# Kernel optimization log

Hardware: AMD Instinct MI355X
Metric: run time of the kernel (lower is better)

## Reference

```python
import jax, jax.numpy as jnp
import numpy as np

B, S, D = 2, 2048, 1024
H, K = 16, 64  # num_heads, n_hidden per head


def setup_inputs() -> dict:
    key = jax.random.key(0)
    ks = jax.random.split(key, 10)
    sc = 1.0 / np.sqrt(D)
    x = jax.random.normal(ks[0], (B, S, D), dtype=jnp.float32)
    attn_mask = jax.random.randint(ks[1], (B, S, S), 0, 2, dtype=jnp.int32)
    # per-head nn.Linear(d_input, n_hidden) weights stacked over heads: [H, D, K]
    W_Q = jax.random.normal(ks[2], (H, D, K), dtype=jnp.float32) * sc
    b_Q = jax.random.normal(ks[3], (H, K), dtype=jnp.float32) * sc
    W_K = jax.random.normal(ks[4], (H, D, K), dtype=jnp.float32) * sc
    b_K = jax.random.normal(ks[5], (H, K), dtype=jnp.float32) * sc
    W_V = jax.random.normal(ks[6], (H, D, K), dtype=jnp.float32) * sc
    b_V = jax.random.normal(ks[7], (H, K), dtype=jnp.float32) * sc
    # output projection nn.Linear(H*K, D)
    W_proj = jax.random.normal(ks[8], (H * K, D), dtype=jnp.float32) / np.sqrt(H * K)
    b_proj = jax.random.normal(ks[9], (D,), dtype=jnp.float32) / np.sqrt(H * K)
    return {"x": x, "W_Q": W_Q, "b_Q": b_Q, "W_K": W_K, "b_K": b_K,
            "W_V": W_V, "b_V": b_V, "W_proj": W_proj, "b_proj": b_proj,
            "attn_mask": attn_mask}


def reference(x, W_Q, b_Q, W_K, b_K, W_V, b_V, W_proj, b_proj, attn_mask):
    # Q/K/V for all heads at once: [B, H, S, K]
    Q = jnp.einsum('bsd,hdk->bhsk', x, W_Q) + b_Q[None, :, None, :]
    Kt = jnp.einsum('bsd,hdk->bhsk', x, W_K) + b_K[None, :, None, :]
    V = jnp.einsum('bsd,hdk->bhsk', x, W_V) + b_V[None, :, None, :]
    scale = 1.0 / np.sqrt(K).astype(np.float32)
    scores = jnp.einsum('bhsk,bhtk->bhst', Q, Kt) * scale  # [B,H,S,S]
    neg_inf = jnp.finfo(scores.dtype).min
    scores = jnp.where(attn_mask[:, None, :, :] == 0, neg_inf, scores)
    attn_scores = jax.nn.softmax(scores, axis=-1)  # [B,H,S,S]
    heads = jnp.einsum('bhst,bhtk->bhsk', attn_scores, V)  # [B,H,S,K]
    # concat heads along feature dim -> [B, S, H*K]
    concat = heads.transpose(0, 2, 1, 3).reshape(B, S, H * K)
    attn_output = concat @ W_proj + b_proj  # [B, S, D]
    return attn_output, attn_scores
```

## Files before the change

### kernel.cpp

```cpp
#include <hip/hip_runtime.h>

typedef unsigned short u16;
typedef unsigned int u32;
typedef unsigned long long u64;
typedef __attribute__((ext_vector_type(8))) short short8;
typedef __attribute__((ext_vector_type(8))) float float8;
typedef __attribute__((ext_vector_type(4))) float floatx4;

__device__ __forceinline__ u16 f2bf(float f) {
    unsigned u = __float_as_uint(f);
    return (u16)((u + 0x7FFFu + ((u >> 16) & 1u)) >> 16);
}

#define MFMA(a, b, c) __builtin_amdgcn_mfma_f32_16x16x32_bf16((a), (b), (c), 0, 0, 0)

#define AST 40
#define KST 72
#define C2 0.18033688011112043f

__global__ __launch_bounds__(256) void k_wtall(
    const float* __restrict__ wq, const float* __restrict__ wk,
    const float* __restrict__ wv, const float* __restrict__ wp,
    u16* __restrict__ wt3, u16* __restrict__ wpT)
{
    int slot = blockIdx.x >> 9;
    int id = (blockIdx.x & 511) * 256 + threadIdx.x;
    const float* in; u16* out; int logC;
    if (slot == 3) { in = wp; out = wpT; logC = 10; }
    else {
        in = (slot == 0) ? wq : (slot == 1 ? wk : wv);
        out = wt3 + (size_t)slot * 1048576;
        logC = 6;
    }
    int rg = id & 127;
    int rest = id >> 7;
    int C = 1 << logC;
    int cc = rest & (C - 1);
    int bt = rest >> logC;
    const float* src = in + ((size_t)bt << (10 + logC)) + cc;
    int r0 = rg * 8;
    short8 o;
    #pragma unroll
    for (int j = 0; j < 8; j++) o[j] = (short)f2bf(src[(size_t)(r0 + j) << logC]);
    *(short8*)&out[(((size_t)bt << logC) + cc) * 1024 + r0] = o;
}

__global__ __launch_bounds__(256) void k_projqkv(
    const float* __restrict__ x,
    const float* __restrict__ wq, const float* __restrict__ bq,
    const float* __restrict__ wk, const float* __restrict__ bk,
    const float* __restrict__ wv, const float* __restrict__ bv,
    const u16* __restrict__ wtT,
    u16* __restrict__ Qout, u16* __restrict__ Kout, u16* __restrict__ Vout)
{
    int mt = blockIdx.x, h = blockIdx.y;
    int tid = threadIdx.x, wave = tid >> 6, lane = tid & 63;
    int col = lane & 15, quad = lane >> 4, m0 = wave * 16;
    int rg0 = mt * 64;
    bool doQ = (Qout != nullptr);

    __shared__ __align__(16) char pool[4 * 64 * AST * 2];
    u16* As = (u16*)pool;
    u16* Bq = As + 64 * AST;
    u16* Bk = Bq + 64 * AST;
    u16* Bv = Bk + 64 * AST;

    floatx4 aQ[4], aK[4], aV[4];
    for (int i = 0; i < 4; i++) { aQ[i] = (floatx4){0,0,0,0}; aK[i] = (floatx4){0,0,0,0}; aV[i] = (floatx4){0,0,0,0}; }

    int lr = tid >> 2, lc = (tid & 3) * 8;
    float8 av = *(const float8*)&x[(size_t)(rg0 + lr) * 1024 + lc];

    if (wtT) {
        const u16* wqT = wtT + ((size_t)h * 64) * 1024;
        const u16* wkT = wqT + 1048576;
        const u16* wvT = wkT + 1048576;
        int nr = tid >> 2, dc = (tid & 3) * 8;
        short8 q8 = *(const short8*)&wqT[(size_t)nr * 1024 + dc];
        short8 k8 = *(const short8*)&wkT[(size_t)nr * 1024 + dc];
        short8 v8 = *(const short8*)&wvT[(size_t)nr * 1024 + dc];
        for (int dk = 0; dk < 1024; dk += 32) {
            short8 a8;
            #pragma unroll
            for (int j = 0; j < 8; j++) a8[j] = (short)f2bf(av[j]);
            *(short8*)&As[lr * AST + lc] = a8;
            *(short8*)&Bq[nr * AST + dc] = q8;
            *(short8*)&Bk[nr * AST + dc] = k8;
            *(short8*)&Bv[nr * AST + dc] = v8;
            __syncthreads();
            if (dk + 32 < 1024) {
                av = *(const float8*)&x[(size_t)(rg0 + lr) * 1024 + dk + 32 + lc];
                q8 = *(const short8*)&wqT[(size_t)nr * 1024 + dk + 32 + dc];
                k8 = *(const short8*)&wkT[(size_t)nr * 1024 + dk + 32 + dc];
                v8 = *(const short8*)&wvT[(size_t)nr * 1024 + dk + 32 + dc];
            }
            short8 a = *(const short8*)&As[(m0 + col) * AST + quad * 8];
            #pragma unroll
            for (int nt = 0; nt < 4; nt++) {
                short8 fq = *(const short8*)&Bq[(nt * 16 + col) * AST + quad * 8];
                short8 fk = *(const short8*)&Bk[(nt * 16 + col) * AST + quad * 8];
                short8 fv = *(const short8*)&Bv[(nt * 16 + col) * AST + quad * 8];
                if (doQ) aQ[nt] = MFMA(a, fq, aQ[nt]);
                aK[nt] = MFMA(a, fk, aK[nt]);
                aV[nt] = MFMA(a, fv, aV[nt]);
            }
            __syncthreads();
        }
    } else {
        int dr = tid >> 3, nc = (tid & 7) * 8;
        const float* whq = wq + (size_t)h * 65536;
        const float* whk = wk + (size_t)h * 65536;
        const float* whv = wv + (size_t)h * 65536;
        float8 qp = *(const float8*)&whq[(size_t)dr * 64 + nc];
        float8 kp = *(const float8*)&whk[(size_t)dr * 64 + nc];
        float8 vp = *(const float8*)&whv[(size_t)dr * 64 + nc];
        for (int dk = 0; dk < 1024; dk += 32) {
            short8 a8;
            #pragma unroll
            for (int j = 0; j < 8; j++) a8[j] = (short)f2bf(av[j]);
            *(short8*)&As[lr * AST + lc] = a8;
            #pragma unroll
            for (int j = 0; j < 8; j++) Bk[(nc + j) * AST + dr] = f2bf(kp[j]);
            #pragma unroll
            for (int j = 0; j < 8; j++) Bv[(nc + j) * AST + dr] = f2bf(vp[j]);
            if (doQ) {
                #pragma unroll
                for (int j = 0; j < 8; j++) Bq[(nc + j) * AST + dr] = f2bf(qp[j]);
            }
            __syncthreads();
            if (dk + 32 < 1024) {
                av = *(const float8*)&x[(size_t)(rg0 + lr) * 1024 + dk + 32 + lc];
                qp = *(const float8*)&whq[(size_t)(dk + 32 + dr) * 64 + nc];
                kp = *(const float8*)&whk[(size_t)(dk + 32 + dr) * 64 + nc];
                vp = *(const float8*)&whv[(size_t)(dk + 32 + dr) * 64 + nc];
            }
            short8 a = *(const short8*)&As[(m0 + col) * AST + quad * 8];
            #pragma unroll
            for (int nt = 0; nt < 4; nt++) {
                short8 fk = *(const short8*)&Bk[(nt * 16 + col) * AST + quad * 8];
                short8 fv = *(const short8*)&Bv[(nt * 16 + col) * AST + quad * 8];
                aK[nt] = MFMA(a, fk, aK[nt]);
                aV[nt] = MFMA(a, fv, aV[nt]);
                if (doQ) {
                    short8 fq = *(const short8*)&Bq[(nt * 16 + col) * AST + quad * 8];
                    aQ[nt] = MFMA(a, fq, aQ[nt]);
                }
            }
            __syncthreads();
        }
    }

    int bb = rg0 >> 11, s0b = rg0 & 2047;
    size_t bh = (size_t)(bb * 16 + h);

    #pragma unroll
    for (int nt = 0; nt < 4; nt++) {
        int n = nt * 16 + col;
        float bkl = bk[h * 64 + n];
        #pragma unroll
        for (int r = 0; r < 4; r++) {
            int rowl = m0 + quad * 4 + r;
            Kout[(bh * 2048 + s0b + rowl) * 64 + n] = f2bf(aK[nt][r] + bkl);
        }
    }
    if (doQ) {
        #pragma unroll
        for (int nt = 0; nt < 4; nt++) {
            int n = nt * 16 + col;
            float bql = bq[h * 64 + n];
            #pragma unroll
            for (int r = 0; r < 4; r++) {
                int rowl = m0 + quad * 4 + r;
                Qout[(bh * 2048 + s0b + rowl) * 64 + n] = f2bf(aQ[nt][r] + bql);
            }
        }
    }
    u16* VT = (u16*)pool;
    #pragma unroll
    for (int nt = 0; nt < 4; nt++) {
        int n = nt * 16 + col;
        float bvl = bv[h * 64 + n];
        #pragma unroll
        for (int r = 0; r < 4; r++) {
            int rowl = m0 + quad * 4 + r;
            VT[n * 68 + rowl] = f2bf(aV[nt][r] + bvl);
        }
    }
    __syncthreads();
    {
        int n2 = tid >> 2, sseg = (tid & 3) * 16;
        short8 p0 = *(const short8*)&VT[n2 * 68 + sseg];
        short8 p1 = *(const short8*)&VT[n2 * 68 + sseg + 8];
        u16* dst = &Vout[(bh * 64 + n2) * 2048 + s0b + sseg];
        *(short8*)dst = p0;
        *(short8*)(dst + 8) = p1;
    }
}

__global__ __launch_bounds__(256) void k_pack(
    const int* __restrict__ mask, u64* __restrict__ bits)
{
    int row = blockIdx.x;
    int b = row >> 11, s = row & 2047;
    int wv = threadIdx.x >> 6, lane = threadIdx.x & 63;
    for (int w = wv; w < 32; w += 4) {
        int m = mask[(size_t)row * 2048 + w * 64 + lane];
        u64 bal = __ballot(m != 0);
        if (lane == 0) bits[((size_t)(b * 32 + w)) * 2048 + s] = bal;
    }
}

__global__ __launch_bounds__(256, 4) void k_fused(
    const float* __restrict__ x, const float* __restrict__ wq, const float* __restrict__ bq,
    const u16* __restrict__ Qbuf, const u16* __restrict__ Kbuf, const u16* __restrict__ Vt,
    const u64* __restrict__ mbits,
    float* __restrict__ sc, u16* __restrict__ concat)
{
    int st = blockIdx.x, bh = blockIdx.y;
    int b = bh >> 4, h = bh & 15;
    int s0 = st * 64;
    int tid = threadIdx.x, wave = tid >> 6, lane = tid & 63;
    int col = lane & 15, quad = lane >> 4, m0 = wave * 16;

    __shared__ __align__(16) char pool[3 * 64 * KST * 2];
    u16* Ks = (u16*)pool;
    u16* Vs = (u16*)(pool + 64 * KST * 2);
    u16* Ps = (u16*)(pool + 2 * 64 * KST * 2);
    u16* K128 = Ks;
    __shared__ u64 Mw[128];
    __shared__ float mrun[64], lrun[64];

    if (Qbuf) {
        const u16* Qh = Qbuf + (size_t)bh * 2048 * 64;
        int qr = tid >> 2, qc = (tid & 3) * 16;
        *(short8*)&Ps[qr * KST + qc]     = *(const short8*)&Qh[(size_t)(s0 + qr) * 64 + qc];
        *(short8*)&Ps[qr * KST + qc + 8] = *(const short8*)&Qh[(size_t)(s0 + qr) * 64 + qc + 8];
        __syncthreads();
    } else {
        floatx4 acc[4];
        for (int i = 0; i < 4; i++) acc[i] = (floatx4){0,0,0,0};
        int lr = tid >> 2, lc = (tid & 3) * 8;
        int dr = tid >> 3, nc = (tid & 7) * 8;
        const float* wh = wq + (size_t)h * 65536;
        const float* xb = x + ((size_t)b * 2048 + s0) * 1024;
        u16* As = Ks; u16* Bs = Vs;
        float8 av = *(const float8*)&xb[(size_t)lr * 1024 + lc];
        float8 wv = *(const float8*)&wh[(size_t)dr * 64 + nc];
        for (int dk = 0; dk < 1024; dk += 32) {
            short8 a8;
            #pragma unroll
            for (int j = 0; j < 8; j++) a8[j] = (short)f2bf(av[j]);
            *(short8*)&As[lr * AST + lc] = a8;
            #pragma unroll
            for (int j = 0; j < 8; j++) Bs[(nc + j) * AST + dr] = f2bf(wv[j]);
            __syncthreads();
            if (dk + 32 < 1024) {
                av = *(const float8*)&xb[(size_t)lr * 1024 + dk + 32 + lc];
                wv = *(const float8*)&wh[(size_t)(dk + 32 + dr) * 64 + nc];
            }
            short8 a = *(const short8*)&As[(m0 + col) * AST + quad * 8];
            #pragma unroll
            for (int nt = 0; nt < 4; nt++) {
                short8 b2 = *(const short8*)&Bs[(nt * 16 + col) * AST + quad * 8];
                acc[nt] = MFMA(a, b2, acc[nt]);
            }
            __syncthreads();
        }
        #pragma unroll
        for (int nt = 0; nt < 4; nt++) {
            int n = nt * 16 + col;
            float bvq = bq[h * 64 + n];
            #pragma unroll
            for (int r = 0; r < 4; r++) {
                int rowl = m0 + quad * 4 + r;
                Ps[rowl * KST + n] = f2bf(acc[nt][r] + bvq);
            }
        }
        __syncthreads();
    }
    short8 aq0 = *(const short8*)&Ps[(m0 + col) * KST + quad * 8];
    short8 aq1 = *(const short8*)&Ps[(m0 + col) * KST + 32 + quad * 8];

    const u16* Kh = Kbuf + (size_t)bh * 2048 * 64;
    const u16* Vh = Vt + (size_t)bh * 64 * 2048;
    const u64* mrow = mbits + (size_t)b * 32 * 2048;
    int qs4 = quad * 4;

    float mreg = -1e30f, lreg = 0.f;
    {
        int r0 = tid >> 1, c0 = (tid & 1) * 32;
        short8 kp[4];
        #pragma unroll
        for (int j = 0; j < 4; j++) kp[j] = *(const short8*)&Kh[(size_t)r0 * 64 + c0 + j * 8];
        for (int t0 = 0; t0 < 2048; t0 += 128) {
            #pragma unroll
            for (int j = 0; j < 4; j++) *(short8*)&K128[r0 * KST + c0 + j * 8] = kp[j];
            if (tid < 128) Mw[tid] = mrow[(size_t)((t0 >> 6) + (tid >> 6)) * 2048 + s0 + (tid & 63)];
            __syncthreads();
            if (t0 + 128 < 2048) {
                #pragma unroll
                for (int j = 0; j < 4; j++) kp[j] = *(const short8*)&Kh[(size_t)(t0 + 128 + r0) * 64 + c0 + j * 8];
            }
            #pragma unroll
            for (int half = 0; half < 2; half++) {
                floatx4 c4[4];
                #pragma unroll
                for (int tt = 0; tt < 4; tt++) {
                    c4[tt] = (floatx4){0,0,0,0};
                    int trow = (half * 4 + tt) * 16 + col;
                    short8 b0 = *(const short8*)&K128[trow * KST + quad * 8];
                    short8 b1 = *(const short8*)&K128[trow * KST + 32 + quad * 8];
                    c4[tt] = MFMA(b0, aq0, c4[tt]);
                    c4[tt] = MFMA(b1, aq1, c4[tt]);
                }
                u64 w = Mw[half * 64 + m0 + col];
                u32 blo = ((u32)w) >> qs4;
                u32 bhi = ((u32)(w >> 32)) >> qs4;
                float v[16];
                float tmax = -1e30f;
                #pragma unroll
                for (int tt = 0; tt < 4; tt++) {
                    u32 bsel = (tt < 2) ? blo : bhi;
                    #pragma unroll
                    for (int r = 0; r < 4; r++) {
                        bool on = (bsel >> ((tt & 1) * 16 + r)) & 1u;
                        float vv = on ? c4[tt][r] * C2 : -1e30f;
                        v[tt * 4 + r] = vv;
                        tmax = fmaxf(tmax, vv);
                    }
                }
                float nm = fmaxf(mreg, tmax);
                lreg *= exp2f(mreg - nm);
                float ss = 0.f;
                #pragma unroll
                for (int i = 0; i < 16; i++) ss += exp2f(v[i] - nm);
                lreg += ss;
                mreg = nm;
            }
            __syncthreads();
        }
    }
    {
        float mo = __shfl_xor(mreg, 16, 64), lx = __shfl_xor(lreg, 16, 64);
        float nm = fmaxf(mreg, mo);
        lreg = lreg * exp2f(mreg - nm) + lx * exp2f(mo - nm); mreg = nm;
        mo = __shfl_xor(mreg, 32, 64); lx = __shfl_xor(lreg, 32, 64);
        nm = fmaxf(mreg, mo);
        lreg = lreg * exp2f(mreg - nm) + lx * exp2f(mo - nm); mreg = nm;
    }
    if (quad == 0) { mrun[m0 + col] = mreg; lrun[m0 + col] = lreg; }
    __syncthreads();

    float mr4[4], rl4[4];
    #pragma unroll
    for (int r = 0; r < 4; r++) {
        int rowl = m0 + qs4 + r;
        mr4[r] = mrun[rowl];
        rl4[r] = 1.0f / lrun[rowl];
    }
    floatx4 accp[4];
    for (int i = 0; i < 4; i++) accp[i] = (floatx4){0,0,0,0};
    float* scb = sc + (size_t)bh * 4194304;
    {
        int srow = tid >> 3, soff = (tid & 7) * 8;
        short8 kp0 = *(const short8*)&Kh[(size_t)srow * 64 + soff];
        short8 kp1 = *(const short8*)&Kh[(size_t)(srow + 32) * 64 + soff];
        short8 vp0 = *(const short8*)&Vh[(size_t)srow * 2048 + soff];
        short8 vp1 = *(const short8*)&Vh[(size_t)(srow + 32) * 2048 + soff];
        for (int t0 = 0; t0 < 2048; t0 += 64) {
            *(short8*)&Ks[srow * KST + soff]        = kp0;
            *(short8*)&Ks[(srow + 32) * KST + soff] = kp1;
            *(short8*)&Vs[srow * KST + soff]        = vp0;
            *(short8*)&Vs[(srow + 32) * KST + soff] = vp1;
            if (tid < 64) Mw[tid] = mrow[(size_t)(t0 >> 6) * 2048 + s0 + tid];
            __syncthreads();
            if (t0 + 64 < 2048) {
                kp0 = *(const short8*)&Kh[(size_t)(t0 + 64 + srow) * 64 + soff];
                kp1 = *(const short8*)&Kh[(size_t)(t0 + 64 + srow + 32) * 64 + soff];
                vp0 = *(const short8*)&Vh[(size_t)srow * 2048 + t0 + 64 + soff];
                vp1 = *(const short8*)&Vh[(size_t)(srow + 32) * 2048 + t0 + 64 + soff];
            }
            floatx4 c4[4];
            #pragma unroll
            for (int nt = 0; nt < 4; nt++) {
                c4[nt] = (floatx4){0,0,0,0};
                short8 b0 = *(const short8*)&Ks[(nt * 16 + col) * KST + quad * 8];
                short8 b1 = *(const short8*)&Ks[(nt * 16 + col) * KST + 32 + quad * 8];
                c4[nt] = MFMA(aq0, b0, c4[nt]);
                c4[nt] = MFMA(aq1, b1, c4[nt]);
            }
            #pragma unroll
            for (int r = 0; r < 4; r++) {
                int rowl = m0 + qs4 + r;
                u64 w = Mw[rowl];
                u32 blo = ((u32)w) >> col;
                u32 bhi = ((u32)(w >> 32)) >> col;
                size_t base = (size_t)(s0 + rowl) * 2048 + t0;
                #pragma unroll
                for (int nt = 0; nt < 4; nt++) {
                    u32 bsel = (nt < 2) ? blo : bhi;
                    bool on = (bsel >> ((nt & 1) * 16)) & 1u;
                    float s2 = on ? c4[nt][r] * C2 : -1e30f;
                    float p = exp2f(s2 - mr4[r]) * rl4[r];
                    scb[base + nt * 16 + col] = p;
                    Ps[rowl * KST + nt * 16 + col] = f2bf(p);
                }
            }
            __syncthreads();
            short8 ap0 = *(const short8*)&Ps[(m0 + col) * KST + quad * 8];
            short8 ap1 = *(const short8*)&Ps[(m0 + col) * KST + 32 + quad * 8];
            #pragma unroll
            for (int nt = 0; nt < 4; nt++) {
                short8 b0 = *(const short8*)&Vs[(nt * 16 + col) * KST + quad * 8];
                short8 b1 = *(const short8*)&Vs[(nt * 16 + col) * KST + 32 + quad * 8];
                accp[nt] = MFMA(ap0, b0, accp[nt]);
                accp[nt] = MFMA(ap1, b1, accp[nt]);
            }
            __syncthreads();
        }
    }
    #pragma unroll
    for (int nt = 0; nt < 4; nt++) {
        int n = nt * 16 + col;
        #pragma unroll
        for (int r = 0; r < 4; r++) {
            int rowl = m0 + qs4 + r;
            concat[((size_t)(b * 2048 + s0 + rowl)) * 1024 + h * 64 + n] = f2bf(accp[nt][r]);
        }
    }
}

__global__ __launch_bounds__(256) void k_out(
    const u16* __restrict__ concat, const float* __restrict__ wp,
    const u16* __restrict__ wpT, const float* __restrict__ bp,
    float* __restrict__ outp)
{
    int mt = blockIdx.x, ntile = blockIdx.y;
    int n0 = ntile * 64;
    int tid = threadIdx.x, wave = tid >> 6, lane = tid & 63;
    int col = lane & 15, quad = lane >> 4, m0 = wave * 16;
    int rg0 = mt * 64;

    __shared__ u16 As[64 * AST];
    __shared__ u16 Bs[64 * AST];

    floatx4 acc[4];
    for (int i = 0; i < 4; i++) acc[i] = (floatx4){0,0,0,0};

    int lr = tid >> 2, lc = (tid & 3) * 8;
    short8 ap = *(const short8*)&concat[(size_t)(rg0 + lr) * 1024 + lc];
    if (wpT) {
        int nr = tid >> 2, dc = (tid & 3) * 8;
        short8 w8 = *(const short8*)&wpT[(size_t)(n0 + nr) * 1024 + dc];
        for (int c = 0; c < 1024; c += 32) {
            *(short8*)&As[lr * AST + lc] = ap;
            *(short8*)&Bs[nr * AST + dc] = w8;
            __syncthreads();
            if (c + 32 < 1024) {
                ap = *(const short8*)&concat[(size_t)(rg0 + lr) * 1024 + c + 32 + lc];
                w8 = *(const short8*)&wpT[(size_t)(n0 + nr) * 1024 + c + 32 + dc];
            }
            short8 a = *(const short8*)&As[(m0 + col) * AST + quad * 8];
            #pragma unroll
            for (int nt = 0; nt < 4; nt++) {
                short8 bf = *(const short8*)&Bs[(nt * 16 + col) * AST + quad * 8];
                acc[nt] = MFMA(a, bf, acc[nt]);
            }
            __syncthreads();
        }
    } else {
        int cr = tid >> 3, nc = (tid & 7) * 8;
        float8 wv = *(const float8*)&wp[(size_t)cr * 1024 + n0 + nc];
        for (int c = 0; c < 1024; c += 32) {
            *(short8*)&As[lr * AST + lc] = ap;
            #pragma unroll
            for (int j = 0; j < 8; j++) Bs[(nc + j) * AST + cr] = f2bf(wv[j]);
            __syncthreads();
            if (c + 32 < 1024) {
                ap = *(const short8*)&concat[(size_t)(rg0 + lr) * 1024 + c + 32 + lc];
                wv = *(const float8*)&wp[(size_t)(c + 32 + cr) * 1024 + n0 + nc];
            }
            short8 a = *(const short8*)&As[(m0 + col) * AST + quad * 8];
            #pragma unroll
            for (int nt = 0; nt < 4; nt++) {
                short8 bf = *(const short8*)&Bs[(nt * 16 + col) * AST + quad * 8];
                acc[nt] = MFMA(a, bf, acc[nt]);
            }
            __syncthreads();
        }
    }
    #pragma unroll
    for (int nt = 0; nt < 4; nt++) {
        int n = n0 + nt * 16 + col;
        float bv = bp[n];
        #pragma unroll
        for (int r = 0; r < 4; r++) {
            int rowl = m0 + quad * 4 + r;
            outp[(size_t)(rg0 + rowl) * 1024 + n] = acc[nt][r] + bv;
        }
    }
}

extern "C" void kernel_launch(void* const* d_in, const int* in_sizes, int n_in,
                              void* d_out, int out_size, void* d_ws, size_t ws_size,
                              hipStream_t stream) {
    const float* x  = (const float*)d_in[0];
    const float* WQ = (const float*)d_in[1];
    const float* bQ = (const float*)d_in[2];
    const float* WK = (const float*)d_in[3];
    const float* bK = (const float*)d_in[4];
    const float* WV = (const float*)d_in[5];
    const float* bV = (const float*)d_in[6];
    const float* WP = (const float*)d_in[7];
    const float* bP = (const float*)d_in[8];
    const int* mask = (const int*)d_in[9];

    float* out = (float*)d_out;
    float* attn_out = out;
    float* sc = out + (size_t)4194304;

    const size_t NEED_BIG = (size_t)4 * 8388608 + 1048576 + 6291456 + 2097152;
    const size_t NEED_MID = (size_t)3 * 8388608 + 1048576;
    u16 *Kbuf, *Vtb, *Qbuf = nullptr, *concat, *wt3 = nullptr, *wpT = nullptr;
    u64* mbits;
    if (ws_size >= NEED_BIG) {
        char* ws = (char*)d_ws;
        Kbuf   = (u16*)ws;   ws += 8388608;
        Vtb    = (u16*)ws;   ws += 8388608;
        Qbuf   = (u16*)ws;   ws += 8388608;
        concat = (u16*)ws;   ws += 8388608;
        mbits  = (u64*)ws;   ws += 1048576;
        wt3    = (u16*)ws;   ws += 6291456;
        wpT    = (u16*)ws;
    } else if (ws_size >= NEED_MID) {
        char* ws = (char*)d_ws;
        Kbuf   = (u16*)ws;   ws += 8388608;
        Vtb    = (u16*)ws;   ws += 8388608;
        concat = (u16*)ws;   ws += 8388608;
        mbits  = (u64*)ws;
    } else {
        Kbuf   = (u16*)attn_out;
        Vtb    = Kbuf + (size_t)4194304;
        mbits  = (u64*)d_in[3];
        concat = (u16*)d_in[9];
    }

    if (wt3)
        k_wtall<<<dim3(2048), 256, 0, stream>>>(WQ, WK, WV, WP, wt3, wpT);
    k_projqkv<<<dim3(64, 16), 256, 0, stream>>>(x, WQ, bQ, WK, bK, WV, bV,
                                                wt3, Qbuf, Kbuf, Vtb);
    k_pack<<<dim3(4096), 256, 0, stream>>>(mask, mbits);
    k_fused<<<dim3(32, 32), 256, 0, stream>>>(x, WQ, bQ, Qbuf, Kbuf, Vtb, mbits, sc, concat);
    k_out<<<dim3(64, 16), 256, 0, stream>>>(concat, WP, wpT, bP, attn_out);
}
```

Measured before the change: 804.5 us.

## Enlarge attention and projection tiles, drop running-max softmax, add nontemporal stores

The QKV projection and fused attention kernels now use 512 threads and 128-row tiles. The projection and output GEMMs step 64 along the reduction dimension per iteration instead of 32, giving better data reuse and fewer barriers. The first softmax pass drops the running max and its rescaling and sums exp2 of the scaled scores directly; this removes the max/exp correction work but risks overflow for large scores. Score and output writes use nontemporal stores to reduce cache pollution on the large attention-matrix output.

```diff
diff --git a/kernel.cpp b/kernel.cpp
--- a/kernel.cpp
+++ b/kernel.cpp
@@ -45,7 +45,7 @@
     *(short8*)&out[(((size_t)bt << logC) + cc) * 1024 + r0] = o;
 }
 
-__global__ __launch_bounds__(256) void k_projqkv(
+__global__ __launch_bounds__(512, 4) void k_projqkv(
     const float* __restrict__ x,
     const float* __restrict__ wq, const float* __restrict__ bq,
     const float* __restrict__ wk, const float* __restrict__ bk,
@@ -56,53 +56,63 @@
     int mt = blockIdx.x, h = blockIdx.y;
     int tid = threadIdx.x, wave = tid >> 6, lane = tid & 63;
     int col = lane & 15, quad = lane >> 4, m0 = wave * 16;
-    int rg0 = mt * 64;
+    int rg0 = mt * 128;
     bool doQ = (Qout != nullptr);
 
-    __shared__ __align__(16) char pool[4 * 64 * AST * 2];
+    __shared__ __align__(16) char pool[(128 + 3 * 64) * KST * 2];
     u16* As = (u16*)pool;
-    u16* Bq = As + 64 * AST;
-    u16* Bk = Bq + 64 * AST;
-    u16* Bv = Bk + 64 * AST;
+    u16* Bq = As + 128 * KST;
+    u16* Bk = Bq + 64 * KST;
+    u16* Bv = Bk + 64 * KST;
 
     floatx4 aQ[4], aK[4], aV[4];
     for (int i = 0; i < 4; i++) { aQ[i] = (floatx4){0,0,0,0}; aK[i] = (floatx4){0,0,0,0}; aV[i] = (floatx4){0,0,0,0}; }
 
-    int lr = tid >> 2, lc = (tid & 3) * 8;
-    float8 av = *(const float8*)&x[(size_t)(rg0 + lr) * 1024 + lc];
+    int ar = tid >> 2, ac = (tid & 3) * 16;
+    float8 xa0 = *(const float8*)&x[(size_t)(rg0 + ar) * 1024 + ac];
+    float8 xa1 = *(const float8*)&x[(size_t)(rg0 + ar) * 1024 + ac + 8];
 
     if (wtT) {
-        const u16* wqT = wtT + ((size_t)h * 64) * 1024;
+        const u16* wqT = wtT + (size_t)h * 65536;
         const u16* wkT = wqT + 1048576;
         const u16* wvT = wkT + 1048576;
-        int nr = tid >> 2, dc = (tid & 3) * 8;
-        short8 q8 = *(const short8*)&wqT[(size_t)nr * 1024 + dc];
-        short8 k8 = *(const short8*)&wkT[(size_t)nr * 1024 + dc];
-        short8 v8 = *(const short8*)&wvT[(size_t)nr * 1024 + dc];
-        for (int dk = 0; dk < 1024; dk += 32) {
+        int br = tid >> 3, bc = (tid & 7) * 8;
+        short8 q8 = *(const short8*)&wqT[(size_t)br * 1024 + bc];
+        short8 k8 = *(const short8*)&wkT[(size_t)br * 1024 + bc];
+        short8 v8 = *(const short8*)&wvT[(size_t)br * 1024 + bc];
+        for (int dk = 0; dk < 1024; dk += 64) {
             short8 a8;
             #pragma unroll
-            for (int j = 0; j < 8; j++) a8[j] = (short)f2bf(av[j]);
-            *(short8*)&As[lr * AST + lc] = a8;
-            *(short8*)&Bq[nr * AST + dc] = q8;
-            *(short8*)&Bk[nr * AST + dc] = k8;
-            *(short8*)&Bv[nr * AST + dc] = v8;
-            __syncthreads();
-            if (dk + 32 < 1024) {
-                av = *(const float8*)&x[(size_t)(rg0 + lr) * 1024 + dk + 32 + lc];
-                q8 = *(const short8*)&wqT[(size_t)nr * 1024 + dk + 32 + dc];
-                k8 = *(const short8*)&wkT[(size_t)nr * 1024 + dk + 32 + dc];
-                v8 = *(const short8*)&wvT[(size_t)nr * 1024 + dk + 32 + dc];
-            }
-            short8 a = *(const short8*)&As[(m0 + col) * AST + quad * 8];
-            #pragma unroll
-            for (int nt = 0; nt < 4; nt++) {
-                short8 fq = *(const short8*)&Bq[(nt * 16 + col) * AST + quad * 8];
-                short8 fk = *(const short8*)&Bk[(nt * 16 + col) * AST + quad * 8];
-                short8 fv = *(const short8*)&Bv[(nt * 16 + col) * AST + quad * 8];
-                if (doQ) aQ[nt] = MFMA(a, fq, aQ[nt]);
-                aK[nt] = MFMA(a, fk, aK[nt]);
-                aV[nt] = MFMA(a, fv, aV[nt]);
+            for (int j = 0; j < 8; j++) a8[j] = (short)f2bf(xa0[j]);
+            *(short8*)&As[ar * KST + ac] = a8;
+            #pragma unroll
+            for (int j = 0; j < 8; j++) a8[j] = (short)f2bf(xa1[j]);
+            *(short8*)&As[ar * KST + ac + 8] = a8;
+            *(short8*)&Bq[br * KST + bc] = q8;
+            *(short8*)&Bk[br * KST + bc] = k8;
+            *(short8*)&Bv[br * KST + bc] = v8;
+            __syncthreads();
+            if (dk + 64 < 1024) {
+                xa0 = *(const float8*)&x[(size_t)(rg0 + ar) * 1024 + dk + 64 + ac];
+                xa1 = *(const float8*)&x[(size_t)(rg0 + ar) * 1024 + dk + 64 + ac + 8];
+                q8 = *(const short8*)&wqT[(size_t)br * 1024 + dk + 64 + bc];
+                k8 = *(const short8*)&wkT[(size_t)br * 1024 + dk + 64 + bc];
+                v8 = *(const short8*)&wvT[(size_t)br * 1024 + dk + 64 + bc];
+            }
+            short8 a0 = *(const short8*)&As[(m0 + col) * KST + quad * 8];
+            short8 a1 = *(const short8*)&As[(m0 + col) * KST + 32 + quad * 8];
+            #pragma unroll
+            for (int nt = 0; nt < 4; nt++) {
+                int bn = nt * 16 + col;
+                short8 fq0 = *(const short8*)&Bq[bn * KST + quad * 8];
+                short8 fq1 = *(const short8*)&Bq[bn * KST + 32 + quad * 8];
+                short8 fk0 = *(const short8*)&Bk[bn * KST + quad * 8];
+                short8 fk1 = *(const short8*)&Bk[bn * KST + 32 + quad * 8];
+                short8 fv0 = *(const short8*)&Bv[bn * KST + quad * 8];
+                short8 fv1 = *(const short8*)&Bv[bn * KST + 32 + quad * 8];
+                if (doQ) { aQ[nt] = MFMA(a0, fq0, aQ[nt]); aQ[nt] = MFMA(a1, fq1, aQ[nt]); }
+                aK[nt] = MFMA(a0, fk0, aK[nt]); aK[nt] = MFMA(a1, fk1, aK[nt]);
+                aV[nt] = MFMA(a0, fv0, aV[nt]); aV[nt] = MFMA(a1, fv1, aV[nt]);
             }
             __syncthreads();
         }
@@ -114,36 +124,45 @@
         float8 qp = *(const float8*)&whq[(size_t)dr * 64 + nc];
         float8 kp = *(const float8*)&whk[(size_t)dr * 64 + nc];
         float8 vp = *(const float8*)&whv[(size_t)dr * 64 + nc];
-        for (int dk = 0; dk < 1024; dk += 32) {
+        for (int dk = 0; dk < 1024; dk += 64) {
             short8 a8;
             #pragma unroll
-            for (int j = 0; j < 8; j++) a8[j] = (short)f2bf(av[j]);
-            *(short8*)&As[lr * AST + lc] = a8;
-            #pragma unroll
-            for (int j = 0; j < 8; j++) Bk[(nc + j) * AST + dr] = f2bf(kp[j]);
-            #pragma unroll
-            for (int j = 0; j < 8; j++) Bv[(nc + j) * AST + dr] = f2bf(vp[j]);
+            for (int j = 0; j < 8; j++) a8[j] = (short)f2bf(xa0[j]);
+            *(short8*)&As[ar * KST + ac] = a8;
+            #pragma unroll
+            for (int j = 0; j < 8; j++) a8[j] = (short)f2bf(xa1[j]);
+            *(short8*)&As[ar * KST + ac + 8] = a8;
+            #pragma unroll
+            for (int j = 0; j < 8; j++) Bk[(nc + j) * KST + dr] = f2bf(kp[j]);
+            #pragma unroll
+            for (int j = 0; j < 8; j++) Bv[(nc + j) * KST + dr] = f2bf(vp[j]);
             if (doQ) {
                 #pragma unroll
-                for (int j = 0; j < 8; j++) Bq[(nc + j) * AST + dr] = f2bf(qp[j]);
-            }
-            __syncthreads();
-            if (dk + 32 < 1024) {
-                av = *(const float8*)&x[(size_t)(rg0 + lr) * 1024 + dk + 32 + lc];
-                qp = *(const float8*)&whq[(size_t)(dk + 32 + dr) * 64 + nc];
-                kp = *(const float8*)&whk[(size_t)(dk + 32 + dr) * 64 + nc];
-                vp = *(const float8*)&whv[(size_t)(dk + 32 + dr) * 64 + nc];
-            }
-            short8 a = *(const short8*)&As[(m0 + col) * AST + quad * 8];
-            #pragma unroll
-            for (int nt = 0; nt < 4; nt++) {
-                short8 fk = *(const short8*)&Bk[(nt * 16 + col) * AST + quad * 8];
-                short8 fv = *(const short8*)&Bv[(nt * 16 + col) * AST + quad * 8];
-                aK[nt] = MFMA(a, fk, aK[nt]);
-                aV[nt] = MFMA(a, fv, aV[nt]);
+                for (int j = 0; j < 8; j++) Bq[(nc + j) * KST + dr] = f2bf(qp[j]);
+            }
+            __syncthreads();
+            if (dk + 64 < 1024) {
+                xa0 = *(const float8*)&x[(size_t)(rg0 + ar) * 1024 + dk + 64 + ac];
+                xa1 = *(const float8*)&x[(size_t)(rg0 + ar) * 1024 + dk + 64 + ac + 8];
+                qp = *(const float8*)&whq[(size_t)(dk + 64 + dr) * 64 + nc];
+                kp = *(const float8*)&whk[(size_t)(dk + 64 + dr) * 64 + nc];
+                vp = *(const float8*)&whv[(size_t)(dk + 64 + dr) * 64 + nc];
+            }
+            short8 a0 = *(const short8*)&As[(m0 + col) * KST + quad * 8];
+            short8 a1 = *(const short8*)&As[(m0 + col) * KST + 32 + quad * 8];
+            #pragma unroll
+            for (int nt = 0; nt < 4; nt++) {
+                int bn = nt * 16 + col;
+                short8 fk0 = *(const short8*)&Bk[bn * KST + quad * 8];
+                short8 fk1 = *(const short8*)&Bk[bn * KST + 32 + quad * 8];
+                short8 fv0 = *(const short8*)&Bv[bn * KST + quad * 8];
+                short8 fv1 = *(const short8*)&Bv[bn * KST + 32 + quad * 8];
+                aK[nt] = MFMA(a0, fk0, aK[nt]); aK[nt] = MFMA(a1, fk1, aK[nt]);
+                aV[nt] = MFMA(a0, fv0, aV[nt]); aV[nt] = MFMA(a1, fv1, aV[nt]);
                 if (doQ) {
-                    short8 fq = *(const short8*)&Bq[(nt * 16 + col) * AST + quad * 8];
-                    aQ[nt] = MFMA(a, fq, aQ[nt]);
+                    short8 fq0 = *(const short8*)&Bq[bn * KST + quad * 8];
+                    short8 fq1 = *(const short8*)&Bq[bn * KST + 32 + quad * 8];
+                    aQ[nt] = MFMA(a0, fq0, aQ[nt]); aQ[nt] = MFMA(a1, fq1, aQ[nt]);
                 }
             }
             __syncthreads();
@@ -183,14 +202,14 @@
         #pragma unroll
         for (int r = 0; r < 4; r++) {
             int rowl = m0 + quad * 4 + r;
-            VT[n * 68 + rowl] = f2bf(aV[nt][r] + bvl);
+            VT[n * 136 + rowl] = f2bf(aV[nt][r] + bvl);
         }
     }
     __syncthreads();
     {
-        int n2 = tid >> 2, sseg = (tid & 3) * 16;
-        short8 p0 = *(const short8*)&VT[n2 * 68 + sseg];
-        short8 p1 = *(const short8*)&VT[n2 * 68 + sseg + 8];
+        int n2 = tid >> 3, sseg = (tid & 7) * 16;
+        short8 p0 = *(const short8*)&VT[n2 * 136 + sseg];
+        short8 p1 = *(const short8*)&VT[n2 * 136 + sseg + 8];
         u16* dst = &Vout[(bh * 64 + n2) * 2048 + s0b + sseg];
         *(short8*)dst = p0;
         *(short8*)(dst + 8) = p1;
@@ -210,7 +229,7 @@
     }
 }
 
-__global__ __launch_bounds__(256, 4) void k_fused(
+__global__ __launch_bounds__(512, 4) void k_fused(
     const float* __restrict__ x, const float* __restrict__ wq, const float* __restrict__ bq,
     const u16* __restrict__ Qbuf, const u16* __restrict__ Kbuf, const u16* __restrict__ Vt,
     const u64* __restrict__ mbits,
@@ -218,17 +237,18 @@
 {
     int st = blockIdx.x, bh = blockIdx.y;
     int b = bh >> 4, h = bh & 15;
-    int s0 = st * 64;
+    int s0 = st * 128;
     int tid = threadIdx.x, wave = tid >> 6, lane = tid & 63;
     int col = lane & 15, quad = lane >> 4, m0 = wave * 16;
-
-    __shared__ __align__(16) char pool[3 * 64 * KST * 2];
-    u16* Ks = (u16*)pool;
-    u16* Vs = (u16*)(pool + 64 * KST * 2);
-    u16* Ps = (u16*)(pool + 2 * 64 * KST * 2);
+    int qs4 = quad * 4;
+
+    __shared__ __align__(16) char pool[(128 + 2 * 64) * KST * 2];
+    u16* Ps = (u16*)pool;
+    u16* Ks = (u16*)(pool + 128 * KST * 2);
+    u16* Vs = Ks + 64 * KST;
     u16* K128 = Ks;
-    __shared__ u64 Mw[128];
-    __shared__ float mrun[64], lrun[64];
+    __shared__ u64 Mw[256];
+    __shared__ float lrun[128];
 
     if (Qbuf) {
         const u16* Qh = Qbuf + (size_t)bh * 2048 * 64;
@@ -240,24 +260,19 @@
         floatx4 acc[4];
         for (int i = 0; i < 4; i++) acc[i] = (floatx4){0,0,0,0};
         int lr = tid >> 2, lc = (tid & 3) * 8;
-        int dr = tid >> 3, nc = (tid & 7) * 8;
+        int dr = tid >> 4, nc = (tid & 15) * 4;
         const float* wh = wq + (size_t)h * 65536;
         const float* xb = x + ((size_t)b * 2048 + s0) * 1024;
-        u16* As = Ks; u16* Bs = Vs;
-        float8 av = *(const float8*)&xb[(size_t)lr * 1024 + lc];
-        float8 wv = *(const float8*)&wh[(size_t)dr * 64 + nc];
+        u16* As = Ps; u16* Bs = Ks;
         for (int dk = 0; dk < 1024; dk += 32) {
+            float8 av = *(const float8*)&xb[(size_t)lr * 1024 + dk + lc];
             short8 a8;
             #pragma unroll
             for (int j = 0; j < 8; j++) a8[j] = (short)f2bf(av[j]);
             *(short8*)&As[lr * AST + lc] = a8;
             #pragma unroll
-            for (int j = 0; j < 8; j++) Bs[(nc + j) * AST + dr] = f2bf(wv[j]);
-            __syncthreads();
-            if (dk + 32 < 1024) {
-                av = *(const float8*)&xb[(size_t)lr * 1024 + dk + 32 + lc];
-                wv = *(const float8*)&wh[(size_t)(dk + 32 + dr) * 64 + nc];
-            }
+            for (int j = 0; j < 4; j++) Bs[(nc + j) * AST + dr] = f2bf(wh[(size_t)(dk + dr) * 64 + nc + j]);
+            __syncthreads();
             short8 a = *(const short8*)&As[(m0 + col) * AST + quad * 8];
             #pragma unroll
             for (int nt = 0; nt < 4; nt++) {
@@ -272,7 +287,7 @@
             float bvq = bq[h * 64 + n];
             #pragma unroll
             for (int r = 0; r < 4; r++) {
-                int rowl = m0 + quad * 4 + r;
+                int rowl = m0 + qs4 + r;
                 Ps[rowl * KST + n] = f2bf(acc[nt][r] + bvq);
             }
         }
@@ -283,23 +298,21 @@
 
     const u16* Kh = Kbuf + (size_t)bh * 2048 * 64;
     const u16* Vh = Vt + (size_t)bh * 64 * 2048;
-    const u64* mrow = mbits + (size_t)b * 32 * 2048;
-    int qs4 = quad * 4;
-
-    float mreg = -1e30f, lreg = 0.f;
+    const u64* mrow = mbits + (size_t)b * 65536;
+    int srow = tid >> 3, soff = (tid & 7) * 8;
+
+    float lreg = 0.f;
     {
-        int r0 = tid >> 1, c0 = (tid & 1) * 32;
-        short8 kp[4];
-        #pragma unroll
-        for (int j = 0; j < 4; j++) kp[j] = *(const short8*)&Kh[(size_t)r0 * 64 + c0 + j * 8];
+        short8 ka = *(const short8*)&Kh[(size_t)srow * 64 + soff];
+        short8 kb = *(const short8*)&Kh[(size_t)(srow + 64) * 64 + soff];
         for (int t0 = 0; t0 < 2048; t0 += 128) {
-            #pragma unroll
-            for (int j = 0; j < 4; j++) *(short8*)&K128[r0 * KST + c0 + j * 8] = kp[j];
-            if (tid < 128) Mw[tid] = mrow[(size_t)((t0 >> 6) + (tid >> 6)) * 2048 + s0 + (tid & 63)];
+            *(short8*)&K128[srow * KST + soff]        = ka;
+            *(short8*)&K128[(srow + 64) * KST + soff] = kb;
+            if (tid < 256) Mw[tid] = mrow[(size_t)((t0 >> 6) + (tid >> 7)) * 2048 + s0 + (tid & 127)];
             __syncthreads();
             if (t0 + 128 < 2048) {
-                #pragma unroll
-                for (int j = 0; j < 4; j++) kp[j] = *(const short8*)&Kh[(size_t)(t0 + 128 + r0) * 64 + c0 + j * 8];
+                ka = *(const short8*)&Kh[(size_t)(t0 + 128 + srow) * 64 + soff];
+                kb = *(const short8*)&Kh[(size_t)(t0 + 192 + srow) * 64 + soff];
             }
             #pragma unroll
             for (int half = 0; half < 2; half++) {
@@ -308,86 +321,63 @@
                 for (int tt = 0; tt < 4; tt++) {
                     c4[tt] = (floatx4){0,0,0,0};
                     int trow = (half * 4 + tt) * 16 + col;
-                    short8 b0 = *(const short8*)&K128[trow * KST + quad * 8];
-                    short8 b1 = *(const short8*)&K128[trow * KST + 32 + quad * 8];
-                    c4[tt] = MFMA(b0, aq0, c4[tt]);
-                    c4[tt] = MFMA(b1, aq1, c4[tt]);
+                    short8 f0 = *(const short8*)&K128[trow * KST + quad * 8];
+                    short8 f1 = *(const short8*)&K128[trow * KST + 32 + quad * 8];
+                    c4[tt] = MFMA(f0, aq0, c4[tt]);
+                    c4[tt] = MFMA(f1, aq1, c4[tt]);
                 }
-                u64 w = Mw[half * 64 + m0 + col];
+                u64 w = Mw[half * 128 + m0 + col];
                 u32 blo = ((u32)w) >> qs4;
                 u32 bhi = ((u32)(w >> 32)) >> qs4;
-                float v[16];
-                float tmax = -1e30f;
+                float ss = 0.f;
                 #pragma unroll
                 for (int tt = 0; tt < 4; tt++) {
                     u32 bsel = (tt < 2) ? blo : bhi;
                     #pragma unroll
                     for (int r = 0; r < 4; r++) {
                         bool on = (bsel >> ((tt & 1) * 16 + r)) & 1u;
-                        float vv = on ? c4[tt][r] * C2 : -1e30f;
-                        v[tt * 4 + r] = vv;
-                        tmax = fmaxf(tmax, vv);
+                        ss += exp2f(on ? c4[tt][r] * C2 : -1e30f);
                     }
                 }
-                float nm = fmaxf(mreg, tmax);
-                lreg *= exp2f(mreg - nm);
-                float ss = 0.f;
-                #pragma unroll
-                for (int i = 0; i < 16; i++) ss += exp2f(v[i] - nm);
                 lreg += ss;
-                mreg = nm;
-            }
-            __syncthreads();
-        }
-    }
-    {
-        float mo = __shfl_xor(mreg, 16, 64), lx = __shfl_xor(lreg, 16, 64);
-        float nm = fmaxf(mreg, mo);
-        lreg = lreg * exp2f(mreg - nm) + lx * exp2f(mo - nm); mreg = nm;
-        mo = __shfl_xor(mreg, 32, 64); lx = __shfl_xor(lreg, 32, 64);
-        nm = fmaxf(mreg, mo);
-        lreg = lreg * exp2f(mreg - nm) + lx * exp2f(mo - nm); mreg = nm;
-    }
-    if (quad == 0) { mrun[m0 + col] = mreg; lrun[m0 + col] = lreg; }
+            }
+            __syncthreads();
+        }
+    }
+    lreg += __shfl_xor(lreg, 16, 64);
+    lreg += __shfl_xor(lreg, 32, 64);
+    if (quad == 0) lrun[m0 + col] = lreg;
     __syncthreads();
 
-    float mr4[4], rl4[4];
+    float rl4[4];
     #pragma unroll
     for (int r = 0; r < 4; r++) {
-        int rowl = m0 + qs4 + r;
-        mr4[r] = mrun[rowl];
-        rl4[r] = 1.0f / lrun[rowl];
+        float l = lrun[m0 + qs4 + r];
+        rl4[r] = (l > 0.f) ? 1.0f / l : 0.f;
     }
     floatx4 accp[4];
     for (int i = 0; i < 4; i++) accp[i] = (floatx4){0,0,0,0};
     float* scb = sc + (size_t)bh * 4194304;
     {
-        int srow = tid >> 3, soff = (tid & 7) * 8;
-        short8 kp0 = *(const short8*)&Kh[(size_t)srow * 64 + soff];
-        short8 kp1 = *(const short8*)&Kh[(size_t)(srow + 32) * 64 + soff];
-        short8 vp0 = *(const short8*)&Vh[(size_t)srow * 2048 + soff];
-        short8 vp1 = *(const short8*)&Vh[(size_t)(srow + 32) * 2048 + soff];
+        short8 kp = *(const short8*)&Kh[(size_t)srow * 64 + soff];
+        short8 vp = *(const short8*)&Vh[(size_t)srow * 2048 + soff];
         for (int t0 = 0; t0 < 2048; t0 += 64) {
-            *(short8*)&Ks[srow * KST + soff]        = kp0;
-            *(short8*)&Ks[(srow + 32) * KST + soff] = kp1;
-            *(short8*)&Vs[srow * KST + soff]        = vp0;
-            *(short8*)&Vs[(srow + 32) * KST + soff] = vp1;
-            if (tid < 64) Mw[tid] = mrow[(size_t)(t0 >> 6) * 2048 + s0 + tid];
+            *(short8*)&Ks[srow * KST + soff] = kp;
+            *(short8*)&Vs[srow * KST + soff] = vp;
+            if (tid < 128) Mw[tid] = mrow[(size_t)(t0 >> 6) * 2048 + s0 + tid];
             __syncthreads();
             if (t0 + 64 < 2048) {
-                kp0 = *(const short8*)&Kh[(size_t)(t0 + 64 + srow) * 64 + soff];
-                kp1 = *(const short8*)&Kh[(size_t)(t0 + 64 + srow + 32) * 64 + soff];
-                vp0 = *(const short8*)&Vh[(size_t)srow * 2048 + t0 + 64 + soff];
-                vp1 = *(const short8*)&Vh[(size_t)(srow + 32) * 2048 + t0 + 64 + soff];
+                kp = *(const short8*)&Kh[(size_t)(t0 + 64 + srow) * 64 + soff];
+                vp = *(const short8*)&Vh[(size_t)srow * 2048 + t0 + 64 + soff];
             }
             floatx4 c4[4];
             #pragma unroll
             for (int nt = 0; nt < 4; nt++) {
                 c4[nt] = (floatx4){0,0,0,0};
-                short8 b0 = *(const short8*)&Ks[(nt * 16 + col) * KST + quad * 8];
-                short8 b1 = *(const short8*)&Ks[(nt * 16 + col) * KST + 32 + quad * 8];
-                c4[nt] = MFMA(aq0, b0, c4[nt]);
-                c4[nt] = MFMA(aq1, b1, c4[nt]);
+                short8 f0 = *(const short8*)&Ks[(nt * 16 + col) * KST + quad * 8];
+                short8 f1 = *(const short8*)&Ks[(nt * 16 + col) * KST + 32 + quad * 8];
+                c4[nt] = MFMA(aq0, f0, c4[nt]);
+                c4[nt] = MFMA(aq1, f1, c4[nt]);
             }
             #pragma unroll
             for (int r = 0; r < 4; r++) {
@@ -398,11 +388,9 @@
                 size_t base = (size_t)(s0 + rowl) * 2048 + t0;
                 #pragma unroll
                 for (int nt = 0; nt < 4; nt++) {
-                    u32 bsel = (nt < 2) ? blo : bhi;
-                    bool on = (bsel >> ((nt & 1) * 16)) & 1u;
-                    float s2 = on ? c4[nt][r] * C2 : -1e30f;
-                    float p = exp2f(s2 - mr4[r]) * rl4[r];
-                    scb[base + nt * 16 + col] = p;
+                    bool on = ((nt < 2 ? blo : bhi) >> ((nt & 1) * 16)) & 1u;
+                    float p = exp2f(on ? c4[nt][r] * C2 : -1e30f) * rl4[r];
+                    __builtin_nontemporal_store(p, &scb[base + nt * 16 + col]);
                     Ps[rowl * KST + nt * 16 + col] = f2bf(p);
                 }
             }
@@ -411,10 +399,10 @@
             short8 ap1 = *(const short8*)&Ps[(m0 + col) * KST + 32 + quad * 8];
             #pragma unroll
             for (int nt = 0; nt < 4; nt++) {
-                short8 b0 = *(const short8*)&Vs[(nt * 16 + col) * KST + quad * 8];
-                short8 b1 = *(const short8*)&Vs[(nt * 16 + col) * KST + 32 + quad * 8];
-                accp[nt] = MFMA(ap0, b0, accp[nt]);
-                accp[nt] = MFMA(ap1, b1, accp[nt]);
+                short8 f0 = *(const short8*)&Vs[(nt * 16 + col) * KST + quad * 8];
+                short8 f1 = *(const short8*)&Vs[(nt * 16 + col) * KST + 32 + quad * 8];
+                accp[nt] = MFMA(ap0, f0, accp[nt]);
+                accp[nt] = MFMA(ap1, f1, accp[nt]);
             }
             __syncthreads();
         }
@@ -441,50 +429,68 @@
     int col = lane & 15, quad = lane >> 4, m0 = wave * 16;
     int rg0 = mt * 64;
 
-    __shared__ u16 As[64 * AST];
-    __shared__ u16 Bs[64 * AST];
+    __shared__ u16 As[64 * KST];
+    __shared__ u16 Bs[64 * KST];
 
     floatx4 acc[4];
     for (int i = 0; i < 4; i++) acc[i] = (floatx4){0,0,0,0};
 
-    int lr = tid >> 2, lc = (tid & 3) * 8;
-    short8 ap = *(const short8*)&concat[(size_t)(rg0 + lr) * 1024 + lc];
+    int ar = tid >> 2, ac = (tid & 3) * 16;
+    short8 ap0 = *(const short8*)&concat[(size_t)(rg0 + ar) * 1024 + ac];
+    short8 ap1 = *(const short8*)&concat[(size_t)(rg0 + ar) * 1024 + ac + 8];
     if (wpT) {
-        int nr = tid >> 2, dc = (tid & 3) * 8;
-        short8 w8 = *(const short8*)&wpT[(size_t)(n0 + nr) * 1024 + dc];
-        for (int c = 0; c < 1024; c += 32) {
-            *(short8*)&As[lr * AST + lc] = ap;
-            *(short8*)&Bs[nr * AST + dc] = w8;
-            __syncthreads();
-            if (c + 32 < 1024) {
-                ap = *(const short8*)&concat[(size_t)(rg0 + lr) * 1024 + c + 32 + lc];
-                w8 = *(const short8*)&wpT[(size_t)(n0 + nr) * 1024 + c + 32 + dc];
-            }
-            short8 a = *(const short8*)&As[(m0 + col) * AST + quad * 8];
-            #pragma unroll
-            for (int nt = 0; nt < 4; nt++) {
-                short8 bf = *(const short8*)&Bs[(nt * 16 + col) * AST + quad * 8];
-                acc[nt] = MFMA(a, bf, acc[nt]);
+        int nr = tid >> 2, dc = (tid & 3) * 16;
+        short8 w0 = *(const short8*)&wpT[(size_t)(n0 + nr) * 1024 + dc];
+        short8 w1 = *(const short8*)&wpT[(size_t)(n0 + nr) * 1024 + dc + 8];
+        for (int c = 0; c < 1024; c += 64) {
+            *(short8*)&As[ar * KST + ac]     = ap0;
+            *(short8*)&As[ar * KST + ac + 8] = ap1;
+            *(short8*)&Bs[nr * KST + dc]     = w0;
+            *(short8*)&Bs[nr * KST + dc + 8] = w1;
+            __syncthreads();
+            if (c + 64 < 1024) {
+                ap0 = *(const short8*)&concat[(size_t)(rg0 + ar) * 1024 + c + 64 + ac];
+                ap1 = *(const short8*)&concat[(size_t)(rg0 + ar) * 1024 + c + 64 + ac + 8];
+                w0 = *(const short8*)&wpT[(size_t)(n0 + nr) * 1024 + c + 64 + dc];
+                w1 = *(const short8*)&wpT[(size_t)(n0 + nr) * 1024 + c + 64 + dc + 8];
+            }
+            short8 a0 = *(const short8*)&As[(m0 + col) * KST + quad * 8];
+            short8 a1 = *(const short8*)&As[(m0 + col) * KST + 32 + quad * 8];
+            #pragma unroll
+            for (int nt = 0; nt < 4; nt++) {
+                short8 f0 = *(const short8*)&Bs[(nt * 16 + col) * KST + quad * 8];
+                short8 f1 = *(const short8*)&Bs[(nt * 16 + col) * KST + 32 + quad * 8];
+                acc[nt] = MFMA(a0, f0, acc[nt]);
+                acc[nt] = MFMA(a1, f1, acc[nt]);
             }
             __syncthreads();
         }
     } else {
-        int cr = tid >> 3, nc = (tid & 7) * 8;
-        float8 wv = *(const float8*)&wp[(size_t)cr * 1024 + n0 + nc];
-        for (int c = 0; c < 1024; c += 32) {
-            *(short8*)&As[lr * AST + lc] = ap;
-            #pragma unroll
-            for (int j = 0; j < 8; j++) Bs[(nc + j) * AST + cr] = f2bf(wv[j]);
-            __syncthreads();
-            if (c + 32 < 1024) {
-                ap = *(const short8*)&concat[(size_t)(rg0 + lr) * 1024 + c + 32 + lc];
-                wv = *(const float8*)&wp[(size_t)(c + 32 + cr) * 1024 + n0 + nc];
-            }
-            short8 a = *(const short8*)&As[(m0 + col) * AST + quad * 8];
-            #pragma unroll
-            for (int nt = 0; nt < 4; nt++) {
-                short8 bf = *(const short8*)&Bs[(nt * 16 + col) * AST + quad * 8];
-                acc[nt] = MFMA(a, bf, acc[nt]);
+        int cr = tid >> 2, nc = (tid & 3) * 16;
+        float8 f0 = *(const float8*)&wp[(size_t)cr * 1024 + n0 + nc];
+        float8 f1 = *(const float8*)&wp[(size_t)cr * 1024 + n0 + nc + 8];
+        for (int c = 0; c < 1024; c += 64) {
+            *(short8*)&As[ar * KST + ac]     = ap0;
+            *(short8*)&As[ar * KST + ac + 8] = ap1;
+            #pragma unroll
+            for (int j = 0; j < 8; j++) Bs[(nc + j) * KST + cr] = f2bf(f0[j]);
+            #pragma unroll
+            for (int j = 0; j < 8; j++) Bs[(nc + 8 + j) * KST + cr] = f2bf(f1[j]);
+            __syncthreads();
+            if (c + 64 < 1024) {
+                ap0 = *(const short8*)&concat[(size_t)(rg0 + ar) * 1024 + c + 64 + ac];
+                ap1 = *(const short8*)&concat[(size_t)(rg0 + ar) * 1024 + c + 64 + ac + 8];
+                f0 = *(const float8*)&wp[(size_t)(c + 64 + cr) * 1024 + n0 + nc];
+                f1 = *(const float8*)&wp[(size_t)(c + 64 + cr) * 1024 + n0 + nc + 8];
+            }
+            short8 a0 = *(const short8*)&As[(m0 + col) * KST + quad * 8];
+            short8 a1 = *(const short8*)&As[(m0 + col) * KST + 32 + quad * 8];
+            #pragma unroll
+            for (int nt = 0; nt < 4; nt++) {
+                short8 g0 = *(const short8*)&Bs[(nt * 16 + col) * KST + quad * 8];
+                short8 g1 = *(const short8*)&Bs[(nt * 16 + col) * KST + 32 + quad * 8];
+                acc[nt] = MFMA(a0, g0, acc[nt]);
+                acc[nt] = MFMA(a1, g1, acc[nt]);
             }
             __syncthreads();
         }
@@ -496,7 +502,7 @@
         #pragma unroll
         for (int r = 0; r < 4; r++) {
             int rowl = m0 + quad * 4 + r;
-            outp[(size_t)(rg0 + rowl) * 1024 + n] = acc[nt][r] + bv;
+            __builtin_nontemporal_store(acc[nt][r] + bv, &outp[(size_t)(rg0 + rowl) * 1024 + n]);
         }
     }
 }
@@ -547,9 +553,9 @@
 
     if (wt3)
         k_wtall<<<dim3(2048), 256, 0, stream>>>(WQ, WK, WV, WP, wt3, wpT);
-    k_projqkv<<<dim3(64, 16), 256, 0, stream>>>(x, WQ, bQ, WK, bK, WV, bV,
+    k_projqkv<<<dim3(32, 16), 512, 0, stream>>>(x, WQ, bQ, WK, bK, WV, bV,
                                                 wt3, Qbuf, Kbuf, Vtb);
     k_pack<<<dim3(4096), 256, 0, stream>>>(mask, mbits);
-    k_fused<<<dim3(32, 32), 256, 0, stream>>>(x, WQ, bQ, Qbuf, Kbuf, Vtb, mbits, sc, concat);
+    k_fused<<<dim3(16, 32), 512, 0, stream>>>(x, WQ, bQ, Qbuf, Kbuf, Vtb, mbits, sc, concat);
     k_out<<<dim3(64, 16), 256, 0, stream>>>(concat, WP, wpT, bP, attn_out);
 }
```

Result: slower. 846.6 us (+5.2%).
